# Optimization experiments

Hardware: AMD Instinct MI355X
Metric: run time of the kernel (lower is better)

## Reference

```python
import jax, jax.numpy as jnp
import numpy as np

B, L, D_MODEL, N_HEADS, M = 1, 2048, 512, 8, 128
D_HEAD = D_MODEL // N_HEADS
KERNEL_EPS = 1e-4
DENOM_EPS = 1e-6


def setup_inputs() -> dict:
    key = jax.random.key(0)
    ks = jax.random.split(key, 12)
    s = 0.02  # weight init scale
    return {
        "query": jax.random.normal(ks[0], (B, L, D_MODEL), jnp.float32),
        "key": jax.random.normal(ks[1], (B, L, D_MODEL), jnp.float32),
        "value": jax.random.normal(ks[2], (B, L, D_MODEL), jnp.float32),
        "Wq": jax.random.normal(ks[3], (D_MODEL, D_MODEL), jnp.float32) * s,
        "bq": jnp.zeros((D_MODEL,), jnp.float32),
        "Wk": jax.random.normal(ks[4], (D_MODEL, D_MODEL), jnp.float32) * s,
        "bk": jnp.zeros((D_MODEL,), jnp.float32),
        "Wv": jax.random.normal(ks[5], (D_MODEL, D_MODEL), jnp.float32) * s,
        "bv": jnp.zeros((D_MODEL,), jnp.float32),
        "Wo": jax.random.normal(ks[6], (D_MODEL, D_MODEL), jnp.float32) * s,
        "bo": jnp.zeros((D_MODEL,), jnp.float32),
        # FAVOR+ random feature matrix (d_head, m); treated as a fixed buffer
        "random_features": jax.random.normal(ks[7], (D_HEAD, M), jnp.float32),
    }


def reference(query, key, value, Wq, bq, Wk, bk, Wv, bv, Wo, bo, random_features):
    b, l, _ = query.shape

    def proj_split(x, W, bias):
        # nn.Linear: x @ W.T + b, then split heads -> (b, h, l, d_head)
        y = x @ W.T + bias
        return y.reshape(b, l, N_HEADS, D_HEAD).transpose(0, 2, 1, 3)

    q = proj_split(query, Wq, bq)
    k = proj_split(key, Wk, bk)
    v = proj_split(value, Wv, bv)

    # --- get_projected_queries_and_keys ('exp' kernel) ---
    scale = D_MODEL ** -0.25
    q = q * scale
    k = k * scale
    proj_q = q @ random_features  # (b, h, l, m)
    proj_k = k @ random_features
    h_q = -0.5 * jnp.sum(q * q, axis=-1, keepdims=True)  # (b, h, l, 1)
    h_k = -0.5 * jnp.sum(k * k, axis=-1, keepdims=True)
    # argmax over a size-1 last dim -> stabilizer is h_q itself (faithful to source)
    q_stab = h_q
    k_stab = jnp.max(h_k)  # global max, scalar
    nc = M ** -0.5
    q_prime = nc * (jnp.exp(h_q + (proj_q - q_stab)) + KERNEL_EPS)  # (b, h, l, m)
    k_prime = nc * (jnp.exp(h_k + (proj_k - k_stab)) + KERNEL_EPS)

    # --- causal numerator: per-head cumsum of k' (x) v outer products ---
    head_outs = []
    for h in range(N_HEADS):
        outer = jnp.einsum('blm,bld->blmd', k_prime[:, h], v[:, h])  # (b, l, m, d)
        prefix = jnp.cumsum(outer, axis=1)
        head_outs.append(jnp.einsum('blmd,blm->bld', prefix, q_prime[:, h]))
    numerator = jnp.stack(head_outs, axis=1)  # (b, h, l, d)

    # --- causal denominator: q' . cumsum(k') ---
    denom = jnp.einsum('bhlm,bhlm->bhl', q_prime, jnp.cumsum(k_prime, axis=2))
    context = numerator / (denom[..., None] + DENOM_EPS)

    # unshape and output projection
    context = context.transpose(0, 2, 1, 3).reshape(b, l, D_MODEL)
    return context @ Wo.T + bo
```

## Files before the change

### kernel.cpp

```cpp
#include <hip/hip_runtime.h>
#include <math.h>


#define L       2048
#define DMODEL  512
#define NH      8
#define DH      64
#define M       128
#define CT      64
#define NC      (L/CT)
#define KEPS    1e-4f
#define DEPS    1e-6f
#define SCALE   0.2102241038134286f
#define NCONST  0.08838834764831845f

#define OFF_VB     0
#define OFF_QPB    524288
#define OFF_KPB    1572864
#define OFF_SSB    2621440
#define OFF_SSZ    3670016
#define OFF_CTX    3702784
#define OFF_END    4227072

typedef short bf16x8 __attribute__((ext_vector_type(8)));
typedef float f32x4  __attribute__((ext_vector_type(4)));
typedef __bf16 bf2_t __attribute__((ext_vector_type(2)));
typedef unsigned short ushort_t;

__device__ __forceinline__ ushort_t f2bf(float f) {
    union { __bf16 b; ushort_t u; } cv;
    cv.b = (__bf16)f;
    return cv.u;
}
__device__ __forceinline__ float bf2f(ushort_t u) {
    return __uint_as_float(((unsigned)u) << 16);
}
__device__ __forceinline__ unsigned pack2(float a, float b) {
    bf2_t v;
    v.x = (__bf16)a;
    v.y = (__bf16)b;
    union { bf2_t v; unsigned u; } cv;
    cv.v = v;
    return cv.u;
}

__global__ __launch_bounds__(256) void qkvp_kernel(
    const float* __restrict__ xq, const float* __restrict__ xk, const float* __restrict__ xv,
    const float* __restrict__ Wq, const float* __restrict__ bq,
    const float* __restrict__ Wk, const float* __restrict__ bk,
    const float* __restrict__ Wv, const float* __restrict__ bv,
    const float* __restrict__ RF,
    ushort_t* __restrict__ Vb, ushort_t* __restrict__ QPb, ushort_t* __restrict__ KPb)
{
    __shared__ __align__(16) char smem[24832];
    __shared__ ushort_t Qt[64 * 136];
    __shared__ float ssq[128];
    uint4* As8 = (uint4*)smem;
    uint4* Bs8 = (uint4*)(smem + 520 * 16);
    ushort_t* RFTs = (ushort_t*)smem;

    const int tid  = threadIdx.x;
    const int lane = tid & 63;
    const int wave = tid >> 6;
    const int quad = lane >> 4;
    const int l15  = lane & 15;
    const int z = blockIdx.z;
    const int isK = (z == 1);
    const int row0 = blockIdx.x * 64;
    const int col0 = blockIdx.y * 128;

    const float* X; const float* W; const float* bias;
    if (z == 0)      { X = xq; W = Wq; bias = bq; }
    else if (z == 1) { X = xk; W = Wk; bias = bk; }
    else             { X = xv; W = Wv; bias = bv; }

    f32x4 acc[4][2];
    const f32x4 z4 = {0.f, 0.f, 0.f, 0.f};
    #pragma unroll
    for (int i = 0; i < 4; ++i) { acc[i][0] = z4; acc[i][1] = z4; }

    uint4 ra[2], rb[4];
    auto loadA = [&](int ck) {
        #pragma unroll
        for (int it = 0; it < 2; ++it) {
            int t = tid + it * 256;
            int row = t >> 3, k8 = t & 7;
            const float4* gp = (const float4*)&X[(row0 + row) * DMODEL + ck * 64 + k8 * 8];
            float4 v0 = gp[0], v1 = gp[1];
            ra[it] = make_uint4(pack2(v0.x, v0.y), pack2(v0.z, v0.w),
                                pack2(v1.x, v1.y), pack2(v1.z, v1.w));
        }
    };
    auto loadB = [&](int ck) {
        #pragma unroll
        for (int it = 0; it < 4; ++it) {
            int t = tid + it * 256;
            int col = t >> 3, k8 = t & 7;
            const float4* gp = (const float4*)&W[(col0 + col) * DMODEL + ck * 64 + k8 * 8];
            float4 v0 = gp[0], v1 = gp[1];
            rb[it] = make_uint4(pack2(v0.x, v0.y), pack2(v0.z, v0.w),
                                pack2(v1.x, v1.y), pack2(v1.z, v1.w));
        }
    };

    loadA(0); loadB(0);
    const int wn = wave;
    for (int ck = 0; ck < 8; ++ck) {
        __syncthreads();
        #pragma unroll
        for (int it = 0; it < 2; ++it) {
            int t = tid + it * 256;
            As8[(t & 7) * 65 + (t >> 3)] = ra[it];
        }
        #pragma unroll
        for (int it = 0; it < 4; ++it) {
            int t = tid + it * 256;
            Bs8[(t & 7) * 129 + (t >> 3)] = rb[it];
        }
        __syncthreads();
        if (ck < 7) { loadA(ck + 1); loadB(ck + 1); }
        const bf16x8* Av = (const bf16x8*)As8;
        const bf16x8* Bv = (const bf16x8*)Bs8;
        #pragma unroll
        for (int kc = 0; kc < 2; ++kc) {
            const int k8 = kc * 4 + quad;
            bf16x8 af[4], bfr[2];
            #pragma unroll
            for (int i = 0; i < 4; ++i) af[i] = Av[k8 * 65 + i * 16 + l15];
            #pragma unroll
            for (int j = 0; j < 2; ++j) bfr[j] = Bv[k8 * 129 + wn * 32 + j * 16 + l15];
            #pragma unroll
            for (int i = 0; i < 4; ++i)
                #pragma unroll
                for (int j = 0; j < 2; ++j)
                    acc[i][j] = __builtin_amdgcn_mfma_f32_16x16x32_bf16(af[i], bfr[j], acc[i][j], 0, 0, 0);
        }
    }

    if (z == 2) {
        #pragma unroll
        for (int i = 0; i < 4; ++i)
            #pragma unroll
            for (int j = 0; j < 2; ++j) {
                int c = col0 + wn * 32 + j * 16 + l15;
                float bv_ = bias[c];
                #pragma unroll
                for (int reg = 0; reg < 4; ++reg) {
                    int r = row0 + i * 16 + quad * 4 + reg;
                    Vb[r * DMODEL + c] = f2bf(acc[i][j][reg] + bv_);
                }
            }
        return;
    }

    #pragma unroll
    for (int i = 0; i < 4; ++i)
        #pragma unroll
        for (int j = 0; j < 2; ++j) {
            int c = wn * 32 + j * 16 + l15;
            float bv_ = bias[col0 + c];
            #pragma unroll
            for (int reg = 0; reg < 4; ++reg) {
                int r = i * 16 + quad * 4 + reg;
                Qt[r * 136 + c] = f2bf(acc[i][j][reg] + bv_);
            }
        }
    __syncthreads();

    {
        int m = tid & 127, half = tid >> 7;
        #pragma unroll
        for (int j = 0; j < 32; ++j) {
            int d = half * 32 + j;
            RFTs[m * 72 + d] = f2bf(SCALE * RF[d * M + m]);
        }
    }
    if (isK && tid < 128) {
        int hh = tid >> 6, row = tid & 63;
        float s = 0.f;
        #pragma unroll
        for (int d = 0; d < DH; ++d) {
            float v = bf2f(Qt[row * 136 + hh * 64 + d]);
            s += v * v;
        }
        ssq[tid] = s;
    }
    __syncthreads();

    const int hh = wave >> 1, mh = wave & 1;
    const float s2h = 0.5f * SCALE * SCALE;
    f32x4 pac[4][4];
    #pragma unroll
    for (int i = 0; i < 4; ++i)
        #pragma unroll
        for (int j = 0; j < 4; ++j) pac[i][j] = z4;
    #pragma unroll
    for (int kc = 0; kc < 2; ++kc) {
        bf16x8 af[4], bfr[4];
        #pragma unroll
        for (int i = 0; i < 4; ++i)
            af[i] = *(const bf16x8*)&Qt[(i * 16 + l15) * 136 + hh * 64 + kc * 32 + quad * 8];
        #pragma unroll
        for (int j = 0; j < 4; ++j)
            bfr[j] = *(const bf16x8*)&RFTs[(mh * 64 + j * 16 + l15) * 72 + kc * 32 + quad * 8];
        #pragma unroll
        for (int i = 0; i < 4; ++i)
            #pragma unroll
            for (int j = 0; j < 4; ++j)
                pac[i][j] = __builtin_amdgcn_mfma_f32_16x16x32_bf16(af[i], bfr[j], pac[i][j], 0, 0, 0);
    }

    ushort_t* dst = isK ? KPb : QPb;
    const int hgl = blockIdx.y * 2 + hh;
    #pragma unroll
    for (int i = 0; i < 4; ++i)
        #pragma unroll
        for (int reg = 0; reg < 4; ++reg) {
            int row = i * 16 + quad * 4 + reg;
            float off = isK ? (-s2h * ssq[hh * 64 + row]) : 0.f;
            #pragma unroll
            for (int j = 0; j < 4; ++j) {
                int m = mh * 64 + j * 16 + l15;
                float p = pac[i][j][reg] + off;
                dst[((long)hgl * L + row0 + row) * M + m] = f2bf(NCONST * (__expf(p) + KEPS));
            }
        }
}

__global__ __launch_bounds__(256) void out_gemm_kernel(
    const ushort_t* __restrict__ ctxb, const float* __restrict__ Wo,
    const float* __restrict__ bo, float* __restrict__ out)
{
    __shared__ uint4 As8[8 * 33];
    __shared__ uint4 Bs8[8 * 129];
    const int tid  = threadIdx.x;
    const int lane = tid & 63;
    const int wn   = tid >> 6;
    const int quad = lane >> 4;
    const int l15  = lane & 15;
    const int row0 = blockIdx.x * 32;
    const int col0 = blockIdx.y * 128;

    f32x4 acc[2][2];
    const f32x4 z4 = {0.f, 0.f, 0.f, 0.f};
    acc[0][0] = z4; acc[0][1] = z4; acc[1][0] = z4; acc[1][1] = z4;

    uint4 ra, rb[4];
    auto loadA = [&](int ck) {
        int row = tid >> 3, k8 = tid & 7;
        ra = *(const uint4*)&ctxb[(row0 + row) * DMODEL + ck * 64 + k8 * 8];
    };
    auto loadB = [&](int ck) {
        #pragma unroll
        for (int it = 0; it < 4; ++it) {
            int t = tid + it * 256;
            int col = t >> 3, k8 = t & 7;
            const float4* gp = (const float4*)&Wo[(col0 + col) * DMODEL + ck * 64 + k8 * 8];
            float4 v0 = gp[0], v1 = gp[1];
            rb[it] = make_uint4(pack2(v0.x, v0.y), pack2(v0.z, v0.w),
                                pack2(v1.x, v1.y), pack2(v1.z, v1.w));
        }
    };

    loadA(0); loadB(0);
    for (int ck = 0; ck < 8; ++ck) {
        __syncthreads();
        As8[(tid & 7) * 33 + (tid >> 3)] = ra;
        #pragma unroll
        for (int it = 0; it < 4; ++it) {
            int t = tid + it * 256;
            Bs8[(t & 7) * 129 + (t >> 3)] = rb[it];
        }
        __syncthreads();
        if (ck < 7) { loadA(ck + 1); loadB(ck + 1); }
        const bf16x8* Av = (const bf16x8*)As8;
        const bf16x8* Bv = (const bf16x8*)Bs8;
        #pragma unroll
        for (int kc = 0; kc < 2; ++kc) {
            const int k8 = kc * 4 + quad;
            bf16x8 af[2], bfr[2];
            af[0] = Av[k8 * 33 + l15];
            af[1] = Av[k8 * 33 + 16 + l15];
            #pragma unroll
            for (int j = 0; j < 2; ++j) bfr[j] = Bv[k8 * 129 + wn * 32 + j * 16 + l15];
            #pragma unroll
            for (int i = 0; i < 2; ++i)
                #pragma unroll
                for (int j = 0; j < 2; ++j)
                    acc[i][j] = __builtin_amdgcn_mfma_f32_16x16x32_bf16(af[i], bfr[j], acc[i][j], 0, 0, 0);
        }
    }
    #pragma unroll
    for (int i = 0; i < 2; ++i)
        #pragma unroll
        for (int j = 0; j < 2; ++j) {
            int c = col0 + wn * 32 + j * 16 + l15;
            float bv_ = bo[c];
            #pragma unroll
            for (int reg = 0; reg < 4; ++reg) {
                int r = row0 + i * 16 + quad * 4 + reg;
                out[r * DMODEL + c] = acc[i][j][reg] + bv_;
            }
        }
}

__global__ __launch_bounds__(256) void chunksum_mfma_kernel(
    const ushort_t* __restrict__ KPb, const ushort_t* __restrict__ Vb,
    ushort_t* __restrict__ SSb, float* __restrict__ SSz)
{
    __shared__ ushort_t Kt[128 * 72];
    __shared__ ushort_t Vt[80 * 72];
    const int tid = threadIdx.x;
    const int c = blockIdx.x, h = blockIdx.y;
    const int lane = tid & 63;
    const int wave = tid >> 6;
    const int quad = lane >> 4, l15 = lane & 15;
    const int t = lane, g = wave;

    {
        const ushort_t* kr = &KPb[((long)(h * L) + c * CT + t) * M];
        #pragma unroll
        for (int it = 0; it < 4; ++it) {
            int mo = it * 4 + g;
            uint4 u = *(const uint4*)&kr[mo * 8];
            ushort_t e[8] = {(ushort_t)(u.x & 0xffff), (ushort_t)(u.x >> 16),
                             (ushort_t)(u.y & 0xffff), (ushort_t)(u.y >> 16),
                             (ushort_t)(u.z & 0xffff), (ushort_t)(u.z >> 16),
                             (ushort_t)(u.w & 0xffff), (ushort_t)(u.w >> 16)};
            #pragma unroll
            for (int j = 0; j < 8; ++j) Kt[(mo * 8 + j) * 72 + t] = e[j];
        }
        const ushort_t* vr = &Vb[(c * CT + t) * DMODEL + h * DH];
        #pragma unroll
        for (int it = 0; it < 2; ++it) {
            int dd = it * 4 + g;
            uint4 u = *(const uint4*)&vr[dd * 8];
            ushort_t e[8] = {(ushort_t)(u.x & 0xffff), (ushort_t)(u.x >> 16),
                             (ushort_t)(u.y & 0xffff), (ushort_t)(u.y >> 16),
                             (ushort_t)(u.z & 0xffff), (ushort_t)(u.z >> 16),
                             (ushort_t)(u.w & 0xffff), (ushort_t)(u.w >> 16)};
            #pragma unroll
            for (int j = 0; j < 8; ++j) Vt[(dd * 8 + j) * 72 + t] = e[j];
        }
        if (g == 0) Vt[64 * 72 + t] = 0x3F80;
        if (g == 1) {
            #pragma unroll
            for (int r = 65; r < 80; ++r) Vt[r * 72 + t] = 0;
        }
    }
    __syncthreads();

    f32x4 acc[2][5];
    const f32x4 z4 = {0.f, 0.f, 0.f, 0.f};
    #pragma unroll
    for (int i = 0; i < 2; ++i)
        #pragma unroll
        for (int j = 0; j < 5; ++j) acc[i][j] = z4;
    #pragma unroll
    for (int kt = 0; kt < 2; ++kt) {
        bf16x8 af[2], bfr[5];
        #pragma unroll
        for (int i = 0; i < 2; ++i)
            af[i] = *(const bf16x8*)&Kt[(wave * 32 + i * 16 + l15) * 72 + kt * 32 + quad * 8];
        #pragma unroll
        for (int j = 0; j < 5; ++j)
            bfr[j] = *(const bf16x8*)&Vt[(j * 16 + l15) * 72 + kt * 32 + quad * 8];
        #pragma unroll
        for (int i = 0; i < 2; ++i)
            #pragma unroll
            for (int j = 0; j < 5; ++j)
                acc[i][j] = __builtin_amdgcn_mfma_f32_16x16x32_bf16(af[i], bfr[j], acc[i][j], 0, 0, 0);
    }
    ushort_t* outS = SSb + (long)(h * NC + c) * 8192;
    #pragma unroll
    for (int i = 0; i < 2; ++i)
        #pragma unroll
        for (int reg = 0; reg < 4; ++reg) {
            int m = wave * 32 + i * 16 + quad * 4 + reg;
            #pragma unroll
            for (int j = 0; j < 4; ++j)
                outS[m * 64 + j * 16 + l15] = f2bf(acc[i][j][reg]);
            if (l15 == 0) SSz[(h * NC + c) * M + m] = acc[i][4][reg];
        }
}

__global__ __launch_bounds__(256) void prefix_kernel(
    ushort_t* __restrict__ SSb, float* __restrict__ SSz)
{
    const int h = blockIdx.y;
    if (blockIdx.x == 32) {
        const int m = threadIdx.x;
        if (m < M) {
            float v[NC];
            #pragma unroll
            for (int c = 0; c < NC; ++c) v[c] = SSz[(h * NC + c) * M + m];
            float run = 0.f;
            #pragma unroll
            for (int c = 0; c < NC; ++c) {
                SSz[(h * NC + c) * M + m] = run;
                run += v[c];
            }
        }
        return;
    }
    const int idx = blockIdx.x * 256 + threadIdx.x;
    ushort_t v[NC];
    #pragma unroll
    for (int c = 0; c < NC; ++c) v[c] = SSb[(long)(h * NC + c) * 8192 + idx];
    float run = 0.f;
    #pragma unroll
    for (int c = 0; c < NC; ++c) {
        SSb[(long)(h * NC + c) * 8192 + idx] = f2bf(run);
        run += bf2f(v[c]);
    }
}

__global__ __launch_bounds__(512) void attn_kernel(
    const ushort_t* __restrict__ QPb, const ushort_t* __restrict__ KPb,
    const ushort_t* __restrict__ Vb, const ushort_t* __restrict__ SSb,
    const float* __restrict__ SSz, ushort_t* __restrict__ ctxb)
{
    __shared__ ushort_t Qp[64 * 136];
    __shared__ ushort_t Kp[64 * 136];
    __shared__ ushort_t St[80 * 136];
    __shared__ ushort_t Vt[80 * 72];
    __shared__ ushort_t Am[64 * 72];
    __shared__ float den[CT];
    const int tid = threadIdx.x;
    const int c = blockIdx.x, h = blockIdx.y;
    const int lane = tid & 63;
    const int wave = tid >> 6;
    const int i  = wave & 3;
    const int nh = wave >> 2;
    const int quad = lane >> 4;
    const int l15  = lane & 15;

    for (int t = tid; t < 2048; t += 512) {
        int mat = t >> 10, r = (t >> 4) & 63, c8 = t & 15;
        const ushort_t* src = mat ? KPb : QPb;
        uint4 u = *(const uint4*)&src[((long)(h * L) + c * CT + r) * M + c8 * 8];
        ushort_t* dst = mat ? Kp : Qp;
        *(uint4*)&dst[r * 136 + c8 * 8] = u;
    }
    {
        int t = tid & 63, dg = tid >> 6;
        uint4 u = *(const uint4*)&Vb[(c * CT + t) * DMODEL + h * DH + dg * 8];
        ushort_t e[8] = {(ushort_t)(u.x & 0xffff), (ushort_t)(u.x >> 16),
                         (ushort_t)(u.y & 0xffff), (ushort_t)(u.y >> 16),
                         (ushort_t)(u.z & 0xffff), (ushort_t)(u.z >> 16),
                         (ushort_t)(u.w & 0xffff), (ushort_t)(u.w >> 16)};
        #pragma unroll
        for (int j = 0; j < 8; ++j) Vt[(dg * 8 + j) * 72 + t] = e[j];
    }
    {
        const ushort_t* ssb = SSb + (long)(h * NC + c) * 8192;
        int m = tid & 127, dg = tid >> 7;
        #pragma unroll
        for (int it = 0; it < 2; ++it) {
            int dd = it * 4 + dg;
            uint4 u = *(const uint4*)&ssb[m * 64 + dd * 8];
            ushort_t e[8] = {(ushort_t)(u.x & 0xffff), (ushort_t)(u.x >> 16),
                             (ushort_t)(u.y & 0xffff), (ushort_t)(u.y >> 16),
                             (ushort_t)(u.z & 0xffff), (ushort_t)(u.z >> 16),
                             (ushort_t)(u.w & 0xffff), (ushort_t)(u.w >> 16)};
            #pragma unroll
            for (int j = 0; j < 8; ++j) St[(dd * 8 + j) * 136 + m] = e[j];
        }
    }
    if (tid < 128) St[64 * 136 + tid] = f2bf(SSz[(h * NC + c) * M + tid]);
    if (tid >= 128 && tid < 192) Vt[64 * 72 + (tid - 128)] = 0x3F80;
    for (int t = tid; t < 15 * 136; t += 512) St[65 * 136 + t] = 0;
    for (int t = tid; t < 15 * 72; t += 512)  Vt[65 * 72 + t] = 0;
    __syncthreads();

    f32x4 acc1[2];
    const f32x4 z4 = {0.f, 0.f, 0.f, 0.f};
    acc1[0] = z4; acc1[1] = z4;
    #pragma unroll
    for (int kt = 0; kt < 4; ++kt) {
        bf16x8 af = *(const bf16x8*)&Qp[(i * 16 + l15) * 136 + kt * 32 + quad * 8];
        #pragma unroll
        for (int jt = 0; jt < 2; ++jt) {
            bf16x8 bf = *(const bf16x8*)&Kp[(nh * 32 + jt * 16 + l15) * 136 + kt * 32 + quad * 8];
            acc1[jt] = __builtin_amdgcn_mfma_f32_16x16x32_bf16(af, bf, acc1[jt], 0, 0, 0);
        }
    }
    #pragma unroll
    for (int jt = 0; jt < 2; ++jt) {
        int col = nh * 32 + jt * 16 + l15;
        #pragma unroll
        for (int reg = 0; reg < 4; ++reg) {
            int row = i * 16 + quad * 4 + reg;
            Am[row * 72 + col] = f2bf((col <= row) ? acc1[jt][reg] : 0.f);
        }
    }
    __syncthreads();

    f32x4 acc2[2], acc3;
    acc2[0] = z4; acc2[1] = z4; acc3 = z4;
    #pragma unroll
    for (int kt = 0; kt < 6; ++kt) {
        bf16x8 af = (kt < 2)
            ? *(const bf16x8*)&Am[(i * 16 + l15) * 72 + kt * 32 + quad * 8]
            : *(const bf16x8*)&Qp[(i * 16 + l15) * 136 + (kt - 2) * 32 + quad * 8];
        #pragma unroll
        for (int jt = 0; jt < 2; ++jt) {
            int n = nh * 32 + jt * 16 + l15;
            bf16x8 bf = (kt < 2)
                ? *(const bf16x8*)&Vt[n * 72 + kt * 32 + quad * 8]
                : *(const bf16x8*)&St[n * 136 + (kt - 2) * 32 + quad * 8];
            acc2[jt] = __builtin_amdgcn_mfma_f32_16x16x32_bf16(af, bf, acc2[jt], 0, 0, 0);
        }
        if (nh == 0) {
            bf16x8 bz = (kt < 2)
                ? *(const bf16x8*)&Vt[(64 + l15) * 72 + kt * 32 + quad * 8]
                : *(const bf16x8*)&St[(64 + l15) * 136 + (kt - 2) * 32 + quad * 8];
            acc3 = __builtin_amdgcn_mfma_f32_16x16x32_bf16(af, bz, acc3, 0, 0, 0);
        }
    }
    if (nh == 0 && l15 == 0) {
        #pragma unroll
        for (int reg = 0; reg < 4; ++reg)
            den[i * 16 + quad * 4 + reg] = acc3[reg];
    }
    __syncthreads();
    #pragma unroll
    for (int jt = 0; jt < 2; ++jt) {
        int d = nh * 32 + jt * 16 + l15;
        #pragma unroll
        for (int reg = 0; reg < 4; ++reg) {
            int row = i * 16 + quad * 4 + reg;
            ctxb[(c * CT + row) * DMODEL + h * DH + d] = f2bf(acc2[jt][reg] / (den[row] + DEPS));
        }
    }
}

extern "C" void kernel_launch(void* const* d_in, const int* in_sizes, int n_in,
                              void* d_out, int out_size, void* d_ws, size_t ws_size,
                              hipStream_t stream)
{
    const float* query = (const float*)d_in[0];
    const float* key_  = (const float*)d_in[1];
    const float* value = (const float*)d_in[2];
    const float* Wq = (const float*)d_in[3];
    const float* bq = (const float*)d_in[4];
    const float* Wk = (const float*)d_in[5];
    const float* bk = (const float*)d_in[6];
    const float* Wv = (const float*)d_in[7];
    const float* bv = (const float*)d_in[8];
    const float* Wo = (const float*)d_in[9];
    const float* bo = (const float*)d_in[10];
    const float* RF = (const float*)d_in[11];

    float* ws = (float*)d_ws;
    ushort_t* Vb   = (ushort_t*)(ws + OFF_VB);
    ushort_t* QPb  = (ushort_t*)(ws + OFF_QPB);
    ushort_t* KPb  = (ushort_t*)(ws + OFF_KPB);
    ushort_t* SSb  = (ushort_t*)(ws + OFF_SSB);
    float* SSz     = ws + OFF_SSZ;
    ushort_t* CTXB = (ushort_t*)(ws + OFF_CTX);

    qkvp_kernel<<<dim3(32, 4, 3), 256, 0, stream>>>(query, key_, value,
                                                    Wq, bq, Wk, bk, Wv, bv, RF,
                                                    Vb, QPb, KPb);
    chunksum_mfma_kernel<<<dim3(NC, 8), 256, 0, stream>>>(KPb, Vb, SSb, SSz);
    prefix_kernel<<<dim3(33, 8), 256, 0, stream>>>(SSb, SSz);
    attn_kernel<<<dim3(NC, 8), 512, 0, stream>>>(QPb, KPb, Vb, SSb, SSz, CTXB);
    out_gemm_kernel<<<dim3(64, 4), 256, 0, stream>>>(CTXB, Wo, bo, (float*)d_out);
}
```

Before: 118.9 us.

## Fuse chunk sums and prefix scan into one sequential chunkscan kernel

Replaces the per-chunk state-sum kernel and the separate prefix-scan kernel with one kernel. Each block owns a head and a 32-wide slice of features and walks all chunks in order, accumulating the running state in MFMA registers and writing the exclusive prefix per chunk, with double-buffered LDS staging. It also stores the state transposed (d-major) so the attention kernel can copy it into LDS with vector stores instead of scattered transposes. This removes one launch and a global read/write pass, but exposes only 32 blocks running a serial 32-step loop, which reduces parallelism.

```diff
diff --git a/kernel.cpp b/kernel.cpp
--- a/kernel.cpp
+++ b/kernel.cpp
@@ -42,6 +42,12 @@
     union { bf2_t v; unsigned u; } cv;
     cv.v = v;
     return cv.u;
+}
+__device__ __forceinline__ void unpack8(uint4 u, ushort_t* e) {
+    e[0] = (ushort_t)(u.x & 0xffff); e[1] = (ushort_t)(u.x >> 16);
+    e[2] = (ushort_t)(u.y & 0xffff); e[3] = (ushort_t)(u.y >> 16);
+    e[4] = (ushort_t)(u.z & 0xffff); e[5] = (ushort_t)(u.z >> 16);
+    e[6] = (ushort_t)(u.w & 0xffff); e[7] = (ushort_t)(u.w >> 16);
 }
 
 __global__ __launch_bounds__(256) void qkvp_kernel(
@@ -227,191 +233,92 @@
         }
 }
 
-__global__ __launch_bounds__(256) void out_gemm_kernel(
-    const ushort_t* __restrict__ ctxb, const float* __restrict__ Wo,
-    const float* __restrict__ bo, float* __restrict__ out)
-{
-    __shared__ uint4 As8[8 * 33];
-    __shared__ uint4 Bs8[8 * 129];
-    const int tid  = threadIdx.x;
-    const int lane = tid & 63;
-    const int wn   = tid >> 6;
-    const int quad = lane >> 4;
-    const int l15  = lane & 15;
-    const int row0 = blockIdx.x * 32;
-    const int col0 = blockIdx.y * 128;
-
-    f32x4 acc[2][2];
-    const f32x4 z4 = {0.f, 0.f, 0.f, 0.f};
-    acc[0][0] = z4; acc[0][1] = z4; acc[1][0] = z4; acc[1][1] = z4;
-
-    uint4 ra, rb[4];
-    auto loadA = [&](int ck) {
-        int row = tid >> 3, k8 = tid & 7;
-        ra = *(const uint4*)&ctxb[(row0 + row) * DMODEL + ck * 64 + k8 * 8];
-    };
-    auto loadB = [&](int ck) {
-        #pragma unroll
-        for (int it = 0; it < 4; ++it) {
-            int t = tid + it * 256;
-            int col = t >> 3, k8 = t & 7;
-            const float4* gp = (const float4*)&Wo[(col0 + col) * DMODEL + ck * 64 + k8 * 8];
-            float4 v0 = gp[0], v1 = gp[1];
-            rb[it] = make_uint4(pack2(v0.x, v0.y), pack2(v0.z, v0.w),
-                                pack2(v1.x, v1.y), pack2(v1.z, v1.w));
-        }
-    };
-
-    loadA(0); loadB(0);
-    for (int ck = 0; ck < 8; ++ck) {
-        __syncthreads();
-        As8[(tid & 7) * 33 + (tid >> 3)] = ra;
-        #pragma unroll
-        for (int it = 0; it < 4; ++it) {
-            int t = tid + it * 256;
-            Bs8[(t & 7) * 129 + (t >> 3)] = rb[it];
-        }
-        __syncthreads();
-        if (ck < 7) { loadA(ck + 1); loadB(ck + 1); }
-        const bf16x8* Av = (const bf16x8*)As8;
-        const bf16x8* Bv = (const bf16x8*)Bs8;
-        #pragma unroll
-        for (int kc = 0; kc < 2; ++kc) {
-            const int k8 = kc * 4 + quad;
-            bf16x8 af[2], bfr[2];
-            af[0] = Av[k8 * 33 + l15];
-            af[1] = Av[k8 * 33 + 16 + l15];
-            #pragma unroll
-            for (int j = 0; j < 2; ++j) bfr[j] = Bv[k8 * 129 + wn * 32 + j * 16 + l15];
-            #pragma unroll
-            for (int i = 0; i < 2; ++i)
-                #pragma unroll
-                for (int j = 0; j < 2; ++j)
-                    acc[i][j] = __builtin_amdgcn_mfma_f32_16x16x32_bf16(af[i], bfr[j], acc[i][j], 0, 0, 0);
-        }
-    }
-    #pragma unroll
-    for (int i = 0; i < 2; ++i)
-        #pragma unroll
-        for (int j = 0; j < 2; ++j) {
-            int c = col0 + wn * 32 + j * 16 + l15;
-            float bv_ = bo[c];
-            #pragma unroll
-            for (int reg = 0; reg < 4; ++reg) {
-                int r = row0 + i * 16 + quad * 4 + reg;
-                out[r * DMODEL + c] = acc[i][j][reg] + bv_;
-            }
-        }
-}
-
-__global__ __launch_bounds__(256) void chunksum_mfma_kernel(
+__global__ __launch_bounds__(256) void chunkscan_kernel(
     const ushort_t* __restrict__ KPb, const ushort_t* __restrict__ Vb,
     ushort_t* __restrict__ SSb, float* __restrict__ SSz)
 {
-    __shared__ ushort_t Kt[128 * 72];
-    __shared__ ushort_t Vt[80 * 72];
-    const int tid = threadIdx.x;
-    const int c = blockIdx.x, h = blockIdx.y;
+    __shared__ ushort_t Kt2[2][32 * 72];
+    __shared__ ushort_t Vt2[2][80 * 72];
+    const int tid  = threadIdx.x;
     const int lane = tid & 63;
     const int wave = tid >> 6;
     const int quad = lane >> 4, l15 = lane & 15;
-    const int t = lane, g = wave;
-
-    {
-        const ushort_t* kr = &KPb[((long)(h * L) + c * CT + t) * M];
-        #pragma unroll
-        for (int it = 0; it < 4; ++it) {
-            int mo = it * 4 + g;
-            uint4 u = *(const uint4*)&kr[mo * 8];
-            ushort_t e[8] = {(ushort_t)(u.x & 0xffff), (ushort_t)(u.x >> 16),
-                             (ushort_t)(u.y & 0xffff), (ushort_t)(u.y >> 16),
-                             (ushort_t)(u.z & 0xffff), (ushort_t)(u.z >> 16),
-                             (ushort_t)(u.w & 0xffff), (ushort_t)(u.w >> 16)};
-            #pragma unroll
-            for (int j = 0; j < 8; ++j) Kt[(mo * 8 + j) * 72 + t] = e[j];
-        }
-        const ushort_t* vr = &Vb[(c * CT + t) * DMODEL + h * DH];
-        #pragma unroll
-        for (int it = 0; it < 2; ++it) {
-            int dd = it * 4 + g;
-            uint4 u = *(const uint4*)&vr[dd * 8];
-            ushort_t e[8] = {(ushort_t)(u.x & 0xffff), (ushort_t)(u.x >> 16),
-                             (ushort_t)(u.y & 0xffff), (ushort_t)(u.y >> 16),
-                             (ushort_t)(u.z & 0xffff), (ushort_t)(u.z >> 16),
-                             (ushort_t)(u.w & 0xffff), (ushort_t)(u.w >> 16)};
-            #pragma unroll
-            for (int j = 0; j < 8; ++j) Vt[(dd * 8 + j) * 72 + t] = e[j];
-        }
-        if (g == 0) Vt[64 * 72 + t] = 0x3F80;
-        if (g == 1) {
-            #pragma unroll
-            for (int r = 65; r < 80; ++r) Vt[r * 72 + t] = 0;
-        }
-    }
-    __syncthreads();
-
-    f32x4 acc[2][5];
+    const int h  = blockIdx.x;
+    const int m0 = blockIdx.y * 32;
+    const int mt = wave & 1;
+    const int dg = wave >> 1;
+    const int nDT = dg ? 2 : 3;
+    const int dt0 = dg ? 3 : 0;
+
+    if (wave == 0) { Vt2[0][64 * 72 + lane] = 0x3F80; Vt2[1][64 * 72 + lane] = 0x3F80; }
+    if (wave == 1) {
+        #pragma unroll
+        for (int r = 65; r < 80; ++r) { Vt2[0][r * 72 + lane] = 0; Vt2[1][r * 72 + lane] = 0; }
+    }
+
+    const int t_ = lane, g_ = wave;
+    uint4 rk, rv0, rv1;
+    auto stage_regs = [&](int c) {
+        rk  = *(const uint4*)&KPb[((long)h * L + c * CT + t_) * M + m0 + g_ * 8];
+        const ushort_t* vr = &Vb[(c * CT + t_) * DMODEL + h * DH];
+        rv0 = *(const uint4*)&vr[g_ * 8];
+        rv1 = *(const uint4*)&vr[(4 + g_) * 8];
+    };
+    auto write_lds = [&](int b) {
+        ushort_t e[8];
+        unpack8(rk, e);
+        #pragma unroll
+        for (int j = 0; j < 8; ++j) Kt2[b][(g_ * 8 + j) * 72 + t_] = e[j];
+        unpack8(rv0, e);
+        #pragma unroll
+        for (int j = 0; j < 8; ++j) Vt2[b][(g_ * 8 + j) * 72 + t_] = e[j];
+        unpack8(rv1, e);
+        #pragma unroll
+        for (int j = 0; j < 8; ++j) Vt2[b][((4 + g_) * 8 + j) * 72 + t_] = e[j];
+    };
+
+    f32x4 acc[3];
     const f32x4 z4 = {0.f, 0.f, 0.f, 0.f};
-    #pragma unroll
-    for (int i = 0; i < 2; ++i)
-        #pragma unroll
-        for (int j = 0; j < 5; ++j) acc[i][j] = z4;
-    #pragma unroll
-    for (int kt = 0; kt < 2; ++kt) {
-        bf16x8 af[2], bfr[5];
-        #pragma unroll
-        for (int i = 0; i < 2; ++i)
-            af[i] = *(const bf16x8*)&Kt[(wave * 32 + i * 16 + l15) * 72 + kt * 32 + quad * 8];
-        #pragma unroll
-        for (int j = 0; j < 5; ++j)
-            bfr[j] = *(const bf16x8*)&Vt[(j * 16 + l15) * 72 + kt * 32 + quad * 8];
-        #pragma unroll
-        for (int i = 0; i < 2; ++i)
-            #pragma unroll
-            for (int j = 0; j < 5; ++j)
-                acc[i][j] = __builtin_amdgcn_mfma_f32_16x16x32_bf16(af[i], bfr[j], acc[i][j], 0, 0, 0);
-    }
-    ushort_t* outS = SSb + (long)(h * NC + c) * 8192;
-    #pragma unroll
-    for (int i = 0; i < 2; ++i)
-        #pragma unroll
-        for (int reg = 0; reg < 4; ++reg) {
-            int m = wave * 32 + i * 16 + quad * 4 + reg;
-            #pragma unroll
-            for (int j = 0; j < 4; ++j)
-                outS[m * 64 + j * 16 + l15] = f2bf(acc[i][j][reg]);
-            if (l15 == 0) SSz[(h * NC + c) * M + m] = acc[i][4][reg];
-        }
-}
-
-__global__ __launch_bounds__(256) void prefix_kernel(
-    ushort_t* __restrict__ SSb, float* __restrict__ SSz)
-{
-    const int h = blockIdx.y;
-    if (blockIdx.x == 32) {
-        const int m = threadIdx.x;
-        if (m < M) {
-            float v[NC];
-            #pragma unroll
-            for (int c = 0; c < NC; ++c) v[c] = SSz[(h * NC + c) * M + m];
-            float run = 0.f;
-            #pragma unroll
-            for (int c = 0; c < NC; ++c) {
-                SSz[(h * NC + c) * M + m] = run;
-                run += v[c];
+    acc[0] = z4; acc[1] = z4; acc[2] = z4;
+
+    stage_regs(0);
+    write_lds(0);
+    for (int c = 0; c < NC; ++c) {
+        const int b = c & 1;
+        if (c < NC - 1) stage_regs(c + 1);
+        __syncthreads();
+        {
+            ushort_t* outS = SSb + (long)(h * NC + c) * 8192;
+            const int m = m0 + mt * 16 + l15;
+            #pragma unroll
+            for (int i = 0; i < 3; ++i) {
+                if (i < nDT) {
+                    const int dt = dt0 + i;
+                    if (dt < 4) {
+                        #pragma unroll
+                        for (int reg = 0; reg < 4; ++reg) {
+                            int d = dt * 16 + quad * 4 + reg;
+                            outS[d * 128 + m] = f2bf(acc[i][reg]);
+                        }
+                    } else if (quad == 0) {
+                        SSz[(h * NC + c) * M + m] = acc[i][0];
+                    }
+                }
             }
         }
-        return;
-    }
-    const int idx = blockIdx.x * 256 + threadIdx.x;
-    ushort_t v[NC];
-    #pragma unroll
-    for (int c = 0; c < NC; ++c) v[c] = SSb[(long)(h * NC + c) * 8192 + idx];
-    float run = 0.f;
-    #pragma unroll
-    for (int c = 0; c < NC; ++c) {
-        SSb[(long)(h * NC + c) * 8192 + idx] = f2bf(run);
-        run += bf2f(v[c]);
+        #pragma unroll
+        for (int kt = 0; kt < 2; ++kt) {
+            bf16x8 bf = *(const bf16x8*)&Kt2[b][(mt * 16 + l15) * 72 + kt * 32 + quad * 8];
+            #pragma unroll
+            for (int i = 0; i < 3; ++i) {
+                if (i < nDT) {
+                    const int dt = dt0 + i;
+                    bf16x8 af = *(const bf16x8*)&Vt2[b][(dt * 16 + l15) * 72 + kt * 32 + quad * 8];
+                    acc[i] = __builtin_amdgcn_mfma_f32_16x16x32_bf16(af, bf, acc[i], 0, 0, 0);
+                }
+            }
+        }
+        if (c < NC - 1) { __syncthreads(); write_lds(b ^ 1); }
     }
 }
 
@@ -445,26 +352,16 @@
     {
         int t = tid & 63, dg = tid >> 6;
         uint4 u = *(const uint4*)&Vb[(c * CT + t) * DMODEL + h * DH + dg * 8];
-        ushort_t e[8] = {(ushort_t)(u.x & 0xffff), (ushort_t)(u.x >> 16),
-                         (ushort_t)(u.y & 0xffff), (ushort_t)(u.y >> 16),
-                         (ushort_t)(u.z & 0xffff), (ushort_t)(u.z >> 16),
-                         (ushort_t)(u.w & 0xffff), (ushort_t)(u.w >> 16)};
+        ushort_t e[8]; unpack8(u, e);
         #pragma unroll
         for (int j = 0; j < 8; ++j) Vt[(dg * 8 + j) * 72 + t] = e[j];
     }
     {
         const ushort_t* ssb = SSb + (long)(h * NC + c) * 8192;
-        int m = tid & 127, dg = tid >> 7;
-        #pragma unroll
-        for (int it = 0; it < 2; ++it) {
-            int dd = it * 4 + dg;
-            uint4 u = *(const uint4*)&ssb[m * 64 + dd * 8];
-            ushort_t e[8] = {(ushort_t)(u.x & 0xffff), (ushort_t)(u.x >> 16),
-                             (ushort_t)(u.y & 0xffff), (ushort_t)(u.y >> 16),
-                             (ushort_t)(u.z & 0xffff), (ushort_t)(u.z >> 16),
-                             (ushort_t)(u.w & 0xffff), (ushort_t)(u.w >> 16)};
-            #pragma unroll
-            for (int j = 0; j < 8; ++j) St[(dd * 8 + j) * 136 + m] = e[j];
+        #pragma unroll
+        for (int t = tid; t < 1024; t += 512) {
+            int dr = t >> 4, seg = t & 15;
+            *(uint4*)&St[dr * 136 + seg * 8] = *(const uint4*)&ssb[dr * 128 + seg * 8];
         }
     }
     if (tid < 128) St[64 * 136 + tid] = f2bf(SSz[(h * NC + c) * M + tid]);
@@ -533,6 +430,83 @@
             ctxb[(c * CT + row) * DMODEL + h * DH + d] = f2bf(acc2[jt][reg] / (den[row] + DEPS));
         }
     }
+}
+
+__global__ __launch_bounds__(256) void out_gemm_kernel(
+    const ushort_t* __restrict__ ctxb, const float* __restrict__ Wo,
+    const float* __restrict__ bo, float* __restrict__ out)
+{
+    __shared__ uint4 As8[8 * 33];
+    __shared__ uint4 Bs8[8 * 129];
+    const int tid  = threadIdx.x;
+    const int lane = tid & 63;
+    const int wn   = tid >> 6;
+    const int quad = lane >> 4;
+    const int l15  = lane & 15;
+    const int row0 = blockIdx.x * 32;
+    const int col0 = blockIdx.y * 128;
+
+    f32x4 acc[2][2];
+    const f32x4 z4 = {0.f, 0.f, 0.f, 0.f};
+    acc[0][0] = z4; acc[0][1] = z4; acc[1][0] = z4; acc[1][1] = z4;
+
+    uint4 ra, rb[4];
+    auto loadA = [&](int ck) {
+        int row = tid >> 3, k8 = tid & 7;
+        ra = *(const uint4*)&ctxb[(row0 + row) * DMODEL + ck * 64 + k8 * 8];
+    };
+    auto loadB = [&](int ck) {
+        #pragma unroll
+        for (int it = 0; it < 4; ++it) {
+            int t = tid + it * 256;
+            int col = t >> 3, k8 = t & 7;
+            const float4* gp = (const float4*)&Wo[(col0 + col) * DMODEL + ck * 64 + k8 * 8];
+            float4 v0 = gp[0], v1 = gp[1];
+            rb[it] = make_uint4(pack2(v0.x, v0.y), pack2(v0.z, v0.w),
+                                pack2(v1.x, v1.y), pack2(v1.z, v1.w));
+        }
+    };
+
+    loadA(0); loadB(0);
+    for (int ck = 0; ck < 8; ++ck) {
+        __syncthreads();
+        As8[(tid & 7) * 33 + (tid >> 3)] = ra;
+        #pragma unroll
+        for (int it = 0; it < 4; ++it) {
+            int t = tid + it * 256;
+            Bs8[(t & 7) * 129 + (t >> 3)] = rb[it];
+        }
+        __syncthreads();
+        if (ck < 7) { loadA(ck + 1); loadB(ck + 1); }
+        const bf16x8* Av = (const bf16x8*)As8;
+        const bf16x8* Bv = (const bf16x8*)Bs8;
+        #pragma unroll
+        for (int kc = 0; kc < 2; ++kc) {
+            const int k8 = kc * 4 + quad;
+            bf16x8 af[2], bfr[2];
+            af[0] = Av[k8 * 33 + l15];
+            af[1] = Av[k8 * 33 + 16 + l15];
+            #pragma unroll
+            for (int j = 0; j < 2; ++j) bfr[j] = Bv[k8 * 129 + wn * 32 + j * 16 + l15];
+            #pragma unroll
+            for (int i = 0; i < 2; ++i)
+                #pragma unroll
+                for (int j = 0; j < 2; ++j)
+                    acc[i][j] = __builtin_amdgcn_mfma_f32_16x16x32_bf16(af[i], bfr[j], acc[i][j], 0, 0, 0);
+        }
+    }
+    #pragma unroll
+    for (int i = 0; i < 2; ++i)
+        #pragma unroll
+        for (int j = 0; j < 2; ++j) {
+            int c = col0 + wn * 32 + j * 16 + l15;
+            float bv_ = bo[c];
+            #pragma unroll
+            for (int reg = 0; reg < 4; ++reg) {
+                int r = row0 + i * 16 + quad * 4 + reg;
+                out[r * DMODEL + c] = acc[i][j][reg] + bv_;
+            }
+        }
 }
 
 extern "C" void kernel_launch(void* const* d_in, const int* in_sizes, int n_in,
@@ -563,8 +537,7 @@
     qkvp_kernel<<<dim3(32, 4, 3), 256, 0, stream>>>(query, key_, value,
                                                     Wq, bq, Wk, bk, Wv, bv, RF,
                                                     Vb, QPb, KPb);
-    chunksum_mfma_kernel<<<dim3(NC, 8), 256, 0, stream>>>(KPb, Vb, SSb, SSz);
-    prefix_kernel<<<dim3(33, 8), 256, 0, stream>>>(SSb, SSz);
-    attn_kernel<<<dim3(NC, 8), 512, 0, stream>>>(QPb, KPb, Vb, SSb, SSz, CTXB);
+    chunkscan_kernel<<<dim3(NH, 4), 256, 0, stream>>>(KPb, Vb, SSb, SSz);
+    attn_kernel<<<dim3(NC, NH), 512, 0, stream>>>(QPb, KPb, Vb, SSb, SSz, CTXB);
     out_gemm_kernel<<<dim3(64, 4), 256, 0, stream>>>(CTXB, Wo, bo, (float*)d_out);
 }
```

New measurement: 141.8 us. +19.3%, slower.
